# Performance work log

Hardware: AMD Instinct MI355X
Metric: run time of the kernel (lower is better)

Reference implementation:

```python
import jax, jax.numpy as jnp
import numpy as np

ML, KS, L = 3, 7, 7  # mL, kernelSize, L = 2*mL+1


def _conv(img, kern, pad, groups=1):
    # img: [N,C,H,W], kern: [O, C//groups, kh, kw]
    return jax.lax.conv_general_dilated(
        img, kern, (1, 1), [(pad, pad), (pad, pad)],
        dimension_numbers=("NCHW", "OIHW", "NCHW"),
        feature_group_count=groups)


def setup_inputs() -> dict:
    key = jax.random.key(0)
    ks = jax.random.split(key, 16)
    B, MU = 64, 256
    lin = lambda k, fi, fo: (jax.random.normal(k, (fi, fo), jnp.float32) / np.sqrt(fi)).astype(jnp.float32)
    return {
        "x": jax.random.normal(ks[0], (B, 1, MU, MU), jnp.float32),
        "f": jax.random.normal(ks[1], (B, 1, MU, MU), jnp.float32),
        "kernelA": jax.random.normal(ks[2], (B, 1, 3, 3), jnp.float32),
        "fc1_w1": lin(ks[3], 9, 200), "fc1_b1": jnp.zeros((200,), jnp.float32),
        "fc1_w2": lin(ks[4], 200, ML * KS * KS), "fc1_b2": jnp.zeros((ML * KS * KS,), jnp.float32),
        "fc2_w1": lin(ks[5], 9, 200), "fc2_b1": jnp.zeros((200,), jnp.float32),
        "fc2_w2": lin(ks[6], 200, ML * ML * KS * KS), "fc2_b2": jnp.zeros((ML * ML * KS * KS,), jnp.float32),
    }


def reference(x, f, kernelA, fc1_w1, fc1_b1, fc1_w2, fc1_b2, fc2_w1, fc2_b1, fc2_w2, fc2_b2):
    B, _, mu, _ = x.shape
    pad = KS // 2

    # residual r = f - A x   (per-sample 3x3 stencil conv, grouped)
    r = f - jax.vmap(lambda xi, ki: _conv(xi[None], ki[None], 1)[0])(x, kernelA)  # [B,1,mu,mu]

    # meta-MLPs produce per-sample dynamic conv kernels from the 3x3 stencil
    kA = kernelA.reshape(B, 9)
    h1 = jax.nn.relu(kA @ fc1_w1 + fc1_b1)
    w1 = (h1 @ fc1_w2 + fc1_b2).reshape(B, ML, 1, KS, KS)
    h2 = jax.nn.relu(kA @ fc2_w1 + fc2_b1)
    w2 = (h2 @ fc2_w2 + fc2_b2).reshape(B, ML, ML, KS, KS)

    # per-sample dynamic convs (batched via vmap)
    G1 = jax.vmap(lambda ri, wi: _conv(ri[None], wi, pad)[0])(r, w1)    # [B,mL,mu,mu]
    G2 = jax.vmap(lambda gi, wi: _conv(gi[None], wi, pad)[0])(G1, w2)   # [B,mL,mu,mu]
    G = jnp.concatenate([r, G1, G2], axis=1)                            # [B,L,mu,mu]

    # S = A G : apply per-sample stencil to each of the L channels (depthwise)
    S = jax.vmap(lambda gi, ki: _conv(gi[None], jnp.broadcast_to(ki[None], (L, 1, 3, 3)), 1, groups=L)[0])(G, kernelA)
    S = S.reshape(B, L, mu * mu)
    Gf = G.reshape(B, L, mu * mu)
    lr = r.reshape(B, mu * mu, 1)

    # normal equations: (S S^T) K = S r, tiny [L,L] solve per sample
    M = jnp.einsum("bln,bmn->blm", S, S)    # [B,L,L]
    b = jnp.matmul(S, lr)                   # [B,L,1]
    K = jnp.linalg.solve(M, b)              # [B,L,1]

    x_new = x + jnp.matmul(K.transpose(0, 2, 1), Gf).reshape(B, 1, mu, mu)
    return x_new
```

## Files before the change

kernel.cpp:

```cpp
#include <hip/hip_runtime.h>

#define MU 256
#define NPIX (MU*MU)
#define ML 3
#define KS 7
#define LCH 7
#define NENT 35
#define RBLK 64

__global__ void mlp_kernel(const float* __restrict__ kernelA,
                           const float* __restrict__ fc1_w1, const float* __restrict__ fc1_b1,
                           const float* __restrict__ fc1_w2, const float* __restrict__ fc1_b2,
                           const float* __restrict__ fc2_w1, const float* __restrict__ fc2_b1,
                           const float* __restrict__ fc2_w2, const float* __restrict__ fc2_b2,
                           float* __restrict__ w1_out, float* __restrict__ w2_out) {
    int b = blockIdx.x;
    int t = threadIdx.x;
    __shared__ float kA[9];
    __shared__ float h1[200], h2[200];
    if (t < 9) kA[t] = kernelA[b*9 + t];
    __syncthreads();
    if (t < 200) {
        float s1 = fc1_b1[t], s2 = fc2_b1[t];
        #pragma unroll
        for (int i = 0; i < 9; ++i) {
            s1 += kA[i] * fc1_w1[i*200 + t];
            s2 += kA[i] * fc2_w1[i*200 + t];
        }
        h1[t] = fmaxf(s1, 0.f);
        h2[t] = fmaxf(s2, 0.f);
    }
    __syncthreads();
    if (t < 147) {
        float s = fc1_b2[t];
        for (int i = 0; i < 200; ++i) s += h1[i] * fc1_w2[i*147 + t];
        w1_out[b*147 + t] = s;
    }
    for (int o = t; o < 441; o += 256) {
        float s = fc2_b2[o];
        for (int i = 0; i < 200; ++i) s += h2[i] * fc2_w2[i*441 + o];
        w2_out[b*441 + o] = s;
    }
}

__global__ __launch_bounds__(256, 4) void residual_kernel(
        const float* __restrict__ x, const float* __restrict__ f,
        const float* __restrict__ kA, float* __restrict__ r) {
    int b = blockIdx.z;
    __shared__ float tile[18][72];
    int tx = threadIdx.x, ty = threadIdx.y;
    int tid = ty*64 + tx;
    float k[9];
    #pragma unroll
    for (int i = 0; i < 9; ++i) k[i] = kA[b*9 + i];
    int x0 = blockIdx.x*64, ysub = blockIdx.y*16;
    const float* xb = x + (size_t)b*NPIX;

    for (int u = tid; u < 18*18; u += 256) {
        int row = u / 18, q4 = u % 18;
        int yy = ysub + row - 1;
        int xx = x0 - 4 + q4*4;
        float4 vv = make_float4(0.f, 0.f, 0.f, 0.f);
        if (yy >= 0 && yy < MU && xx >= 0 && xx < MU)
            vv = *(const float4*)(xb + yy*MU + xx);
        *(float4*)&tile[row][q4*4] = vv;
    }
    __syncthreads();

    int ry = ty*4;
    float S0 = 0.f, S1 = 0.f, S2 = 0.f, S3 = 0.f;
    #pragma unroll
    for (int t = 0; t < 6; ++t) {
        float v0 = tile[ry + t][tx + 3];
        float v1 = tile[ry + t][tx + 4];
        float v2 = tile[ry + t][tx + 5];
        float e0 = v0*k[0] + v1*k[1] + v2*k[2];
        float e1 = v0*k[3] + v1*k[4] + v2*k[5];
        float e2 = v0*k[6] + v1*k[7] + v2*k[8];
        if (t == 0) { S0 += e0; }
        if (t == 1) { S1 += e0; S0 += e1; }
        if (t == 2) { S2 += e0; S1 += e1; S0 += e2; }
        if (t == 3) { S3 += e0; S2 += e1; S1 += e2; }
        if (t == 4) {           S3 += e1; S2 += e2; }
        if (t == 5) {                     S3 += e2; }
    }
    float Sv[4] = {S0, S1, S2, S3};
    #pragma unroll
    for (int dy = 0; dy < 4; ++dy) {
        size_t p = (size_t)b*NPIX + (size_t)(ysub + ry + dy)*MU + x0 + tx;
        r[p] = f[p] - Sv[dy];
    }
}

__global__ __launch_bounds__(256) void conv7_g1(
        const float* __restrict__ r, const float* __restrict__ w1,
        float* __restrict__ G1) {
    int b = blockIdx.z;
    __shared__ float tile[22][136];
    int tx = threadIdx.x;
    int ty = threadIdx.y;
    int tid = ty*64 + tx;
    int x0 = blockIdx.x*128, y0 = blockIdx.y*16;
    const float* rb = r + (size_t)b*NPIX;
    const float* wgt = w1 + (size_t)b*147;

    for (int u = tid; u < 22*34; u += 256) {
        int row = u / 34, q4 = u % 34;
        int yy = y0 + row - 3;
        int xx = x0 - 4 + q4*4;
        float4 vv = make_float4(0.f, 0.f, 0.f, 0.f);
        if (yy >= 0 && yy < MU && xx >= 0 && xx < MU)
            vv = *(const float4*)(rb + yy*MU + xx);
        *(float4*)&tile[row][q4*4] = vv;
    }
    __syncthreads();

    float accA[3][4], accB[3][4];
    #pragma unroll
    for (int co = 0; co < 3; ++co)
        #pragma unroll
        for (int dy = 0; dy < 4; ++dy) { accA[co][dy] = 0.f; accB[co][dy] = 0.f; }

    int ry = ty*4;
    #pragma unroll
    for (int ir = 0; ir < 10; ++ir) {
        float v[10];
        #pragma unroll
        for (int h = 0; h < 5; ++h)
            *(float2*)&v[h*2] = *(float2*)&tile[ry + ir][2*tx + h*2];
        #pragma unroll
        for (int dy = 0; dy < 4; ++dy) {
            int i = ir - dy;
            if (i >= 0 && i <= 6) {
                #pragma unroll
                for (int co = 0; co < 3; ++co)
                    #pragma unroll
                    for (int j = 0; j < 7; ++j) {
                        float w = wgt[(co*7 + i)*7 + j];
                        accA[co][dy] += v[1 + j] * w;
                        accB[co][dy] += v[2 + j] * w;
                    }
            }
        }
    }
    #pragma unroll
    for (int dy = 0; dy < 4; ++dy) {
        size_t p = (size_t)b*3*NPIX + (size_t)(y0 + ry + dy)*MU + x0 + 2*tx;
        #pragma unroll
        for (int co = 0; co < 3; ++co)
            *(float2*)&G1[p + (size_t)co*NPIX] = make_float2(accA[co][dy], accB[co][dy]);
    }
}

__global__ __launch_bounds__(256) void conv7_g2(
        const float* __restrict__ G1, const float* __restrict__ w2,
        float* __restrict__ G2) {
    int b = blockIdx.z;
    __shared__ float tile[3][14][136];
    int tx = threadIdx.x;
    int ty = threadIdx.y;
    int tid = ty*64 + tx;
    int x0 = blockIdx.x*128, y0 = blockIdx.y*8;
    const float* g1b = G1 + (size_t)b*3*NPIX;
    const float* wgt = w2 + (size_t)b*441;

    for (int u = tid; u < 3*14*34; u += 256) {
        int c = u / (14*34);
        int rem = u % (14*34);
        int row = rem / 34, q4 = rem % 34;
        int yy = y0 + row - 3;
        int xx = x0 - 4 + q4*4;
        float4 vv = make_float4(0.f, 0.f, 0.f, 0.f);
        if (yy >= 0 && yy < MU && xx >= 0 && xx < MU)
            vv = *(const float4*)(g1b + (size_t)c*NPIX + yy*MU + xx);
        *(float4*)&tile[c][row][q4*4] = vv;
    }
    __syncthreads();

    float accA[3][2], accB[3][2];
    #pragma unroll
    for (int co = 0; co < 3; ++co)
        #pragma unroll
        for (int dy = 0; dy < 2; ++dy) { accA[co][dy] = 0.f; accB[co][dy] = 0.f; }

    int ry = ty*2;
    #pragma unroll
    for (int c = 0; c < 3; ++c) {
        #pragma unroll
        for (int ir = 0; ir < 8; ++ir) {
            float v[10];
            #pragma unroll
            for (int h = 0; h < 5; ++h)
                *(float2*)&v[h*2] = *(float2*)&tile[c][ry + ir][2*tx + h*2];
            #pragma unroll
            for (int dy = 0; dy < 2; ++dy) {
                int i = ir - dy;
                if (i >= 0 && i <= 6) {
                    #pragma unroll
                    for (int co = 0; co < 3; ++co)
                        #pragma unroll
                        for (int j = 0; j < 7; ++j) {
                            float w = wgt[((co*3 + c)*7 + i)*7 + j];
                            accA[co][dy] += v[1 + j] * w;
                            accB[co][dy] += v[2 + j] * w;
                        }
                }
            }
        }
    }
    #pragma unroll
    for (int dy = 0; dy < 2; ++dy) {
        size_t p = (size_t)b*3*NPIX + (size_t)(y0 + ry + dy)*MU + x0 + 2*tx;
        #pragma unroll
        for (int co = 0; co < 3; ++co)
            *(float2*)&G2[p + (size_t)co*NPIX] = make_float2(accA[co][dy], accB[co][dy]);
    }
}

__global__ __launch_bounds__(256, 4) void reduce_kernel(
        const float* __restrict__ r, const float* __restrict__ G1,
        const float* __restrict__ G2, const float* __restrict__ kA,
        float* __restrict__ partial) {
    int b = blockIdx.z;
    __shared__ float tile[7][18][72];
    __shared__ float wsum[NENT][4];
    int tx = threadIdx.x;
    int ty = threadIdx.y;
    int tid = ty*64 + tx;
    float k[9];
    #pragma unroll
    for (int i = 0; i < 9; ++i) k[i] = kA[b*9 + i];

    const float* srcs[7] = {
        r  + (size_t)b*NPIX,
        G1 + (size_t)b*3*NPIX, G1 + (size_t)b*3*NPIX + NPIX, G1 + (size_t)b*3*NPIX + 2*NPIX,
        G2 + (size_t)b*3*NPIX, G2 + (size_t)b*3*NPIX + NPIX, G2 + (size_t)b*3*NPIX + 2*NPIX
    };

    int x0 = blockIdx.x*64;
    int ysub = blockIdx.y*16;

    #pragma unroll
    for (int c = 0; c < 7; ++c) {
        const float* src = srcs[c];
        for (int u = tid; u < 18*18; u += 256) {
            int row = u / 18, q4 = u % 18;
            int yy = ysub + row - 1;
            int xx = x0 - 4 + q4*4;
            float4 vv = make_float4(0.f, 0.f, 0.f, 0.f);
            if (yy >= 0 && yy < MU && xx >= 0 && xx < MU)
                vv = *(const float4*)(src + yy*MU + xx);
            *(float4*)&tile[c][row][q4*4] = vv;
        }
    }
    __syncthreads();

    float acc[64];
    #pragma unroll
    for (int e = 0; e < 64; ++e) acc[e] = 0.f;

    int ry = ty*4;
    float S_all[7][4];
    #pragma unroll
    for (int c = 0; c < 7; ++c) {
        float S0 = 0.f, S1 = 0.f, S2 = 0.f, S3 = 0.f;
        #pragma unroll
        for (int t = 0; t < 6; ++t) {
            float v0 = tile[c][ry + t][tx + 3];
            float v1 = tile[c][ry + t][tx + 4];
            float v2 = tile[c][ry + t][tx + 5];
            float e0 = v0*k[0] + v1*k[1] + v2*k[2];
            float e1 = v0*k[3] + v1*k[4] + v2*k[5];
            float e2 = v0*k[6] + v1*k[7] + v2*k[8];
            if (t == 0) { S0 += e0; }
            if (t == 1) { S1 += e0; S0 += e1; }
            if (t == 2) { S2 += e0; S1 += e1; S0 += e2; }
            if (t == 3) { S3 += e0; S2 += e1; S1 += e2; }
            if (t == 4) {           S3 += e1; S2 += e2; }
            if (t == 5) {                     S3 += e2; }
        }
        S_all[c][0] = S0; S_all[c][1] = S1; S_all[c][2] = S2; S_all[c][3] = S3;
    }
    #pragma unroll
    for (int dy = 0; dy < 4; ++dy) {
        float rv = tile[0][ry + dy + 1][tx + 4];
        int idx = 0;
        #pragma unroll
        for (int l = 0; l < 7; ++l) {
            #pragma unroll
            for (int m = l; m < 7; ++m) {
                acc[idx] += S_all[l][dy] * S_all[m][dy];
                ++idx;
            }
        }
        #pragma unroll
        for (int l = 0; l < 7; ++l) acc[28 + l] += S_all[l][dy] * rv;
    }

    #pragma unroll
    for (int step = 0; step < 6; ++step) {
        const int mask = 1 << step;
        const int nh = 32 >> step;
        bool hi = (tx & mask) != 0;
        #pragma unroll
        for (int i = 0; i < nh; ++i) {
            float send = hi ? acc[i] : acc[i + nh];
            float got = __shfl_xor(send, mask);
            acc[i] = (hi ? acc[i + nh] : acc[i]) + got;
        }
    }
    int ent = ((tx&1)<<5) | ((tx&2)<<3) | ((tx&4)<<1)
            | ((tx&8)>>1) | ((tx&16)>>3) | ((tx&32)>>5);
    if (ent < NENT) wsum[ent][ty] = acc[0];
    __syncthreads();
    if (tid < NENT) {
        float s = wsum[tid][0] + wsum[tid][1] + wsum[tid][2] + wsum[tid][3];
        int blockLinear = blockIdx.y*4 + blockIdx.x;
        partial[((size_t)b*NENT + tid)*RBLK + blockLinear] = s;
    }
}

__global__ void reduce2_kernel(const float* __restrict__ partial,
                               double* __restrict__ M, double* __restrict__ bv) {
    int b = blockIdx.x;
    int wave = threadIdx.x >> 6;
    int lane = threadIdx.x & 63;
    for (int e = wave; e < NENT; e += 4) {
        const float* p = partial + ((size_t)b*NENT + e)*RBLK;
        double s = (double)p[lane];
        #pragma unroll
        for (int off = 32; off; off >>= 1) s += __shfl_down(s, off);
        if (lane == 0) {
            if (e < 28) M[b*28 + e] = s;
            else        bv[b*7 + (e - 28)] = s;
        }
    }
}

__global__ __launch_bounds__(64, 1) void solve_kernel(
        const double* __restrict__ M, const double* __restrict__ bv,
        float* __restrict__ K, int B) {
    int b = blockIdx.x*64 + threadIdx.x;
    if (b >= B) return;
    double A[7][8];
    int idx = 0;
    #pragma unroll
    for (int l = 0; l < 7; ++l)
        #pragma unroll
        for (int m = l; m < 7; ++m) {
            double v = M[b*28 + idx];
            A[l][m] = v;
            A[m][l] = v;
            ++idx;
        }
    #pragma unroll
    for (int l = 0; l < 7; ++l) A[l][7] = bv[b*7 + l];

    #pragma unroll
    for (int col = 0; col < 7; ++col) {
        int piv = col;
        double mx = fabs(A[col][col]);
        #pragma unroll
        for (int rr = 0; rr < 7; ++rr) {
            if (rr > col) {
                double a = fabs(A[rr][col]);
                if (a > mx) { mx = a; piv = rr; }
            }
        }
        #pragma unroll
        for (int rr = 0; rr < 7; ++rr) {
            if (rr > col) {
                bool c = (rr == piv);
                #pragma unroll
                for (int cc = 0; cc < 8; ++cc) {
                    double t0 = A[col][cc], t1 = A[rr][cc];
                    A[col][cc] = c ? t1 : t0;
                    A[rr][cc]  = c ? t0 : t1;
                }
            }
        }
        double d = A[col][col];
        #pragma unroll
        for (int rr = 0; rr < 7; ++rr) {
            if (rr > col) {
                double fct = A[rr][col] / d;
                #pragma unroll
                for (int cc = 0; cc < 8; ++cc) A[rr][cc] -= fct * A[col][cc];
            }
        }
    }
    double Kv[7];
    #pragma unroll
    for (int rr = 6; rr >= 0; --rr) {
        double s = A[rr][7];
        #pragma unroll
        for (int cc = 0; cc < 7; ++cc)
            if (cc > rr) s -= A[rr][cc] * Kv[cc];
        Kv[rr] = s / A[rr][rr];
    }
    #pragma unroll
    for (int l = 0; l < 7; ++l) K[b*7 + l] = (float)Kv[l];
}

__global__ void update_kernel(const float* __restrict__ x, const float* __restrict__ r,
                              const float* __restrict__ G1, const float* __restrict__ G2,
                              const float* __restrict__ K, float* __restrict__ out) {
    int b = blockIdx.z;
    int p4 = blockIdx.x*256 + threadIdx.x;
    float k0 = K[b*7+0], k1 = K[b*7+1], k2 = K[b*7+2], k3 = K[b*7+3];
    float k4 = K[b*7+4], k5 = K[b*7+5], k6 = K[b*7+6];
    size_t q  = (size_t)b*(NPIX/4) + p4;
    size_t q3 = (size_t)b*3*(NPIX/4) + p4;
    const float4* x4  = (const float4*)x;
    const float4* r4  = (const float4*)r;
    const float4* g14 = (const float4*)G1;
    const float4* g24 = (const float4*)G2;
    float4 xv = x4[q], rv = r4[q];
    float4 a = g14[q3], bb = g14[q3 + NPIX/4], c = g14[q3 + 2*(NPIX/4)];
    float4 d = g24[q3], e  = g24[q3 + NPIX/4], g = g24[q3 + 2*(NPIX/4)];
    float4 o;
    o.x = xv.x + k0*rv.x + k1*a.x + k2*bb.x + k3*c.x + k4*d.x + k5*e.x + k6*g.x;
    o.y = xv.y + k0*rv.y + k1*a.y + k2*bb.y + k3*c.y + k4*d.y + k5*e.y + k6*g.y;
    o.z = xv.z + k0*rv.z + k1*a.z + k2*bb.z + k3*c.z + k4*d.z + k5*e.z + k6*g.z;
    o.w = xv.w + k0*rv.w + k1*a.w + k2*bb.w + k3*c.w + k4*d.w + k5*e.w + k6*g.w;
    ((float4*)out)[q] = o;
}

extern "C" void kernel_launch(void* const* d_in, const int* in_sizes, int n_in,
                              void* d_out, int out_size, void* d_ws, size_t ws_size,
                              hipStream_t stream) {
    const float* x       = (const float*)d_in[0];
    const float* f       = (const float*)d_in[1];
    const float* kernelA = (const float*)d_in[2];
    const float* fc1_w1  = (const float*)d_in[3];
    const float* fc1_b1  = (const float*)d_in[4];
    const float* fc1_w2  = (const float*)d_in[5];
    const float* fc1_b2  = (const float*)d_in[6];
    const float* fc2_w1  = (const float*)d_in[7];
    const float* fc2_b1  = (const float*)d_in[8];
    const float* fc2_w2  = (const float*)d_in[9];
    const float* fc2_b2  = (const float*)d_in[10];
    float* out = (float*)d_out;

    const int B = in_sizes[2] / 9;

    double* Mws = (double*)d_ws;
    double* bws = Mws + (size_t)B*28;
    float*  w1  = (float*)(bws + (size_t)B*7);
    float*  w2  = w1 + (size_t)B*147;
    float*  Kv  = w2 + (size_t)B*441;
    float*  r   = Kv + (size_t)B*7;
    float*  G1  = r  + (size_t)B*NPIX;
    float*  G2  = G1 + (size_t)B*3*NPIX;
    float*  partial = G2 + (size_t)B*3*NPIX;

    dim3 cblk(64, 4);
    dim3 rgrd(MU/64, MU/16, B);
    dim3 g1grd(MU/128, MU/16, B);
    dim3 g2grd(MU/128, MU/8, B);

    hipLaunchKernelGGL(mlp_kernel, dim3(B), dim3(256), 0, stream,
                       kernelA, fc1_w1, fc1_b1, fc1_w2, fc1_b2,
                       fc2_w1, fc2_b1, fc2_w2, fc2_b2, w1, w2);
    hipLaunchKernelGGL(residual_kernel, rgrd, cblk, 0, stream, x, f, kernelA, r);
    hipLaunchKernelGGL(conv7_g1, g1grd, cblk, 0, stream, r, w1, G1);
    hipLaunchKernelGGL(conv7_g2, g2grd, cblk, 0, stream, G1, w2, G2);
    hipLaunchKernelGGL(reduce_kernel, rgrd, cblk, 0, stream, r, G1, G2, kernelA, partial);
    hipLaunchKernelGGL(reduce2_kernel, dim3(B), dim3(256), 0, stream, partial, Mws, bws);
    hipLaunchKernelGGL(solve_kernel, dim3((B + 63)/64), dim3(64), 0, stream, Mws, bws, Kv, B);
    hipLaunchKernelGGL(update_kernel, dim3(NPIX/1024, 1, B), dim3(256), 0, stream,
                       x, r, G1, G2, Kv, out);
}
```

Baseline: 195.0 us.

## Fuse residual computation into the first 7x7 dynamic convolution kernel

Merges the residual kernel and the first dynamic convolution into one kernel. Each block loads an x halo tile, computes the residual r = f - A x for the conv halo region in shared memory, then runs the 7x7 convolution from that tile and writes both r and G1. This removes one launch and the global round trip of r into the conv, at the cost of redundant stencil work on halo pixels and more shared memory per block, which may lower occupancy.

```diff
diff --git a/kernel.cpp b/kernel.cpp
--- a/kernel.cpp
+++ b/kernel.cpp
@@ -43,75 +43,55 @@
     }
 }
 
-__global__ __launch_bounds__(256, 4) void residual_kernel(
+__global__ __launch_bounds__(256) void res_g1_kernel(
         const float* __restrict__ x, const float* __restrict__ f,
-        const float* __restrict__ kA, float* __restrict__ r) {
+        const float* __restrict__ kA, const float* __restrict__ w1,
+        float* __restrict__ r, float* __restrict__ G1) {
     int b = blockIdx.z;
-    __shared__ float tile[18][72];
-    int tx = threadIdx.x, ty = threadIdx.y;
-    int tid = ty*64 + tx;
-    float k[9];
-    #pragma unroll
-    for (int i = 0; i < 9; ++i) k[i] = kA[b*9 + i];
-    int x0 = blockIdx.x*64, ysub = blockIdx.y*16;
-    const float* xb = x + (size_t)b*NPIX;
-
-    for (int u = tid; u < 18*18; u += 256) {
-        int row = u / 18, q4 = u % 18;
-        int yy = ysub + row - 1;
-        int xx = x0 - 4 + q4*4;
-        float4 vv = make_float4(0.f, 0.f, 0.f, 0.f);
-        if (yy >= 0 && yy < MU && xx >= 0 && xx < MU)
-            vv = *(const float4*)(xb + yy*MU + xx);
-        *(float4*)&tile[row][q4*4] = vv;
-    }
-    __syncthreads();
-
-    int ry = ty*4;
-    float S0 = 0.f, S1 = 0.f, S2 = 0.f, S3 = 0.f;
-    #pragma unroll
-    for (int t = 0; t < 6; ++t) {
-        float v0 = tile[ry + t][tx + 3];
-        float v1 = tile[ry + t][tx + 4];
-        float v2 = tile[ry + t][tx + 5];
-        float e0 = v0*k[0] + v1*k[1] + v2*k[2];
-        float e1 = v0*k[3] + v1*k[4] + v2*k[5];
-        float e2 = v0*k[6] + v1*k[7] + v2*k[8];
-        if (t == 0) { S0 += e0; }
-        if (t == 1) { S1 += e0; S0 += e1; }
-        if (t == 2) { S2 += e0; S1 += e1; S0 += e2; }
-        if (t == 3) { S3 += e0; S2 += e1; S1 += e2; }
-        if (t == 4) {           S3 += e1; S2 += e2; }
-        if (t == 5) {                     S3 += e2; }
-    }
-    float Sv[4] = {S0, S1, S2, S3};
-    #pragma unroll
-    for (int dy = 0; dy < 4; ++dy) {
-        size_t p = (size_t)b*NPIX + (size_t)(ysub + ry + dy)*MU + x0 + tx;
-        r[p] = f[p] - Sv[dy];
-    }
-}
-
-__global__ __launch_bounds__(256) void conv7_g1(
-        const float* __restrict__ r, const float* __restrict__ w1,
-        float* __restrict__ G1) {
-    int b = blockIdx.z;
-    __shared__ float tile[22][136];
+    __shared__ float xt[24][144];
+    __shared__ float rt[22][136];
     int tx = threadIdx.x;
     int ty = threadIdx.y;
     int tid = ty*64 + tx;
     int x0 = blockIdx.x*128, y0 = blockIdx.y*16;
-    const float* rb = r + (size_t)b*NPIX;
+    const float* xb = x + (size_t)b*NPIX;
+    const float* fb = f + (size_t)b*NPIX;
     const float* wgt = w1 + (size_t)b*147;
-
-    for (int u = tid; u < 22*34; u += 256) {
-        int row = u / 34, q4 = u % 34;
-        int yy = y0 + row - 3;
-        int xx = x0 - 4 + q4*4;
+    float k[9];
+    #pragma unroll
+    for (int i = 0; i < 9; ++i) k[i] = kA[b*9 + i];
+
+    for (int u = tid; u < 24*36; u += 256) {
+        int row = u / 36, q4 = u % 36;
+        int yy = y0 + row - 4;
+        int xx = x0 - 8 + q4*4;
         float4 vv = make_float4(0.f, 0.f, 0.f, 0.f);
         if (yy >= 0 && yy < MU && xx >= 0 && xx < MU)
-            vv = *(const float4*)(rb + yy*MU + xx);
-        *(float4*)&tile[row][q4*4] = vv;
+            vv = *(const float4*)(xb + yy*MU + xx);
+        *(float4*)&xt[row][q4*4] = vv;
+    }
+    __syncthreads();
+
+    for (int u = tid; u < 22*34; u += 256) {
+        int row = u / 34, c4 = u % 34;
+        int Y = y0 - 3 + row;
+        int X = x0 - 4 + 4*c4;
+        bool inb = (Y >= 0 && Y < MU && X >= 0 && X < MU);
+        float4 fv = make_float4(0.f, 0.f, 0.f, 0.f);
+        if (inb) fv = *(const float4*)(fb + Y*MU + X);
+        float fr[4] = {fv.x, fv.y, fv.z, fv.w};
+        float rr[4];
+        #pragma unroll
+        for (int cc = 0; cc < 4; ++cc) {
+            float s = 0.f;
+            #pragma unroll
+            for (int di = 0; di < 3; ++di)
+                #pragma unroll
+                for (int dj = 0; dj < 3; ++dj)
+                    s += xt[row + di][4*c4 + 3 + cc + dj] * k[di*3 + dj];
+            rr[cc] = inb ? (fr[cc] - s) : 0.f;
+        }
+        *(float4*)&rt[row][4*c4] = make_float4(rr[0], rr[1], rr[2], rr[3]);
     }
     __syncthreads();
 
@@ -127,7 +107,7 @@
         float v[10];
         #pragma unroll
         for (int h = 0; h < 5; ++h)
-            *(float2*)&v[h*2] = *(float2*)&tile[ry + ir][2*tx + h*2];
+            *(float2*)&v[h*2] = *(float2*)&rt[ry + ir][2*tx + h*2];
         #pragma unroll
         for (int dy = 0; dy < 4; ++dy) {
             int i = ir - dy;
@@ -145,6 +125,8 @@
     }
     #pragma unroll
     for (int dy = 0; dy < 4; ++dy) {
+        size_t pr = (size_t)b*NPIX + (size_t)(y0 + ry + dy)*MU + x0 + 2*tx;
+        *(float2*)&r[pr] = *(float2*)&rt[3 + ry + dy][4 + 2*tx];
         size_t p = (size_t)b*3*NPIX + (size_t)(y0 + ry + dy)*MU + x0 + 2*tx;
         #pragma unroll
         for (int co = 0; co < 3; ++co)
@@ -462,8 +444,7 @@
     hipLaunchKernelGGL(mlp_kernel, dim3(B), dim3(256), 0, stream,
                        kernelA, fc1_w1, fc1_b1, fc1_w2, fc1_b2,
                        fc2_w1, fc2_b1, fc2_w2, fc2_b2, w1, w2);
-    hipLaunchKernelGGL(residual_kernel, rgrd, cblk, 0, stream, x, f, kernelA, r);
-    hipLaunchKernelGGL(conv7_g1, g1grd, cblk, 0, stream, r, w1, G1);
+    hipLaunchKernelGGL(res_g1_kernel, g1grd, cblk, 0, stream, x, f, kernelA, w1, r, G1);
     hipLaunchKernelGGL(conv7_g2, g2grd, cblk, 0, stream, G1, w2, G2);
     hipLaunchKernelGGL(reduce_kernel, rgrd, cblk, 0, stream, r, G1, G2, kernelA, partial);
     hipLaunchKernelGGL(reduce2_kernel, dim3(B), dim3(256), 0, stream, partial, Mws, bws);
```

Result: no change. 192.1 us (-1.5%).
